# Kernel tuning notes

Hardware: AMD Instinct MI355X
Metric: run time of the kernel (lower is better)

The kernel has to match this reference:

```python
import jax, jax.numpy as jnp
import numpy as np

EMBEDDING_DIM = 64

def setup_inputs() -> dict:
    key = jax.random.key(0)
    kq, kk, kv = jax.random.split(key, 3)
    shape = (8, 8, 2048, 64)  # [B, H, S, D]
    return {
        "query": jax.random.normal(kq, shape, dtype=jnp.float32),
        "key": jax.random.normal(kk, shape, dtype=jnp.float32),
        "value": jax.random.normal(kv, shape, dtype=jnp.float32),
    }

def reference(query, key, value):
    # dot_product = Q @ K^T over last two dims
    scores = jnp.einsum('bhqd,bhkd->bhqk', query, key)
    # Faithful to source: scaler = d**0.5, then divide by sqrt(scaler) => d**0.25
    scale = jnp.sqrt(jnp.asarray(EMBEDDING_DIM ** 0.5, dtype=scores.dtype))
    attn = jax.nn.softmax(scores / scale, axis=-1)
    return jnp.einsum('bhqk,bhkd->bhqd', attn, value)
```

## Files before the change

### kernel.cpp

```cpp
#include <hip/hip_runtime.h>

typedef _Float16 f16;
typedef _Float16 half8 __attribute__((ext_vector_type(8)));
typedef __fp16 h2 __attribute__((ext_vector_type(2)));
typedef float f32x16 __attribute__((ext_vector_type(16)));
typedef unsigned int u32x2 __attribute__((ext_vector_type(2)));

constexpr int S  = 2048;
constexpr int D  = 64;
constexpr int TQ = 128;
constexpr int TK = 64;
constexpr int KP = 72;
constexpr int VP = 72;
constexpr int TP = 66;
constexpr int HEADS = 64;
constexpr size_t HSZ = (size_t)S * D;
constexpr size_t KG_BYTES = (size_t)HEADS * HSZ * 2;
constexpr float MSUB = 14.0f;

__global__ __launch_bounds__(256) void prep(const float* __restrict__ K,
                                            const float* __restrict__ V,
                                            f16* __restrict__ Kg,
                                            f16* __restrict__ Vt) {
    __shared__ __align__(16) f16 Ts[64 * TP];
    const int t = threadIdx.x;
    const size_t hb = (size_t)blockIdx.y * HSZ;
    const int k0 = blockIdx.x * 64;
    const int row = t >> 2, c = (t & 3) * 16;

    {
        const float* src = K + hb + (size_t)(k0 + row) * D + c;
        f16* dst = Kg + hb + (size_t)(k0 + row) * D + c;
        #pragma unroll
        for (int u = 0; u < 2; ++u) {
            float4 a = *(const float4*)(src + u * 8);
            float4 b = *(const float4*)(src + u * 8 + 4);
            half8 h;
            h[0] = (f16)a.x; h[1] = (f16)a.y; h[2] = (f16)a.z; h[3] = (f16)a.w;
            h[4] = (f16)b.x; h[5] = (f16)b.y; h[6] = (f16)b.z; h[7] = (f16)b.w;
            *(half8*)(dst + u * 8) = h;
        }
    }
    {
        const float* src = V + hb + (size_t)(k0 + row) * D + c;
        f16* dst = &Ts[row * TP + c];
        #pragma unroll
        for (int u = 0; u < 4; ++u) {
            float4 a = *(const float4*)(src + u * 4);
            *(h2*)(dst + u * 4)     = __builtin_amdgcn_cvt_pkrtz(a.x, a.y);
            *(h2*)(dst + u * 4 + 2) = __builtin_amdgcn_cvt_pkrtz(a.z, a.w);
        }
    }
    __syncthreads();
    {
        const int d = row, kc = c;
        f16 tmp[16];
        #pragma unroll
        for (int i = 0; i < 16; ++i) tmp[i] = Ts[(kc + i) * TP + d];
        f16* dst = Vt + hb + (size_t)d * S + k0 + kc;
        *(half8*)dst       = *(half8*)&tmp[0];
        *(half8*)(dst + 8) = *(half8*)&tmp[8];
    }
}

__device__ __forceinline__ u32x2 plswap(unsigned int a, unsigned int b) {
#if __has_builtin(__builtin_amdgcn_permlane32_swap)
    return __builtin_amdgcn_permlane32_swap(a, b, false, false);
#else
    asm volatile("v_permlane32_swap_b32 %0, %1" : "+v"(a), "+v"(b));
    u32x2 r; r[0] = a; r[1] = b; return r;
#endif
}

__global__ __launch_bounds__(256, 4) void attn_fwd(
    const float* __restrict__ Q, const f16* __restrict__ Kg,
    const f16* __restrict__ Vt, float* __restrict__ O)
{
    __shared__ __align__(16) f16 Ks[2][TK * KP];
    __shared__ __align__(16) f16 Vs[2][D * VP];

    const int tid  = threadIdx.x;
    const int w    = tid >> 6;
    const int lane = tid & 63;
    const int l31  = lane & 31;
    const int hi   = lane >> 5;

    const int lid  = blockIdx.y * 16 + blockIdx.x;
    const int phys = (lid & 7) * 128 + (lid >> 3);
    const int head = phys >> 4;
    const int qb   = phys & 15;
    const size_t hb = (size_t)head * HSZ;
    const int qbase = qb * TQ + w * 32;

    const float SCALE = 0.35355339059327373f * 1.44269504088896340f;

    half8 qf[4];
    #pragma unroll
    for (int db = 0; db < 4; ++db) {
        const float* qp = Q + hb + (size_t)(qbase + l31) * D + db * 16 + hi * 8;
        float4 a = *(const float4*)(qp);
        float4 b = *(const float4*)(qp + 4);
        half8 h;
        h[0] = (f16)(a.x * SCALE); h[1] = (f16)(a.y * SCALE);
        h[2] = (f16)(a.z * SCALE); h[3] = (f16)(a.w * SCALE);
        h[4] = (f16)(b.x * SCALE); h[5] = (f16)(b.y * SCALE);
        h[6] = (f16)(b.z * SCALE); h[7] = (f16)(b.w * SCALE);
        qf[db] = h;
    }

    f32x16 minit;
    #pragma unroll
    for (int r = 0; r < 16; ++r) minit[r] = -MSUB;

    half8 onesB;
    #pragma unroll
    for (int r = 0; r < 8; ++r) onesB[r] = (f16)1.0f;

    f32x16 accO[2];
    f32x16 accL;
    #pragma unroll
    for (int r = 0; r < 16; ++r) { accO[0][r] = 0.0f; accO[1][r] = 0.0f; accL[r] = 0.0f; }

    const int srow = tid >> 2, sc = (tid & 3) * 16;
    const f16* Kg0 = Kg + hb + (size_t)srow * D + sc;
    const f16* Vg0 = Vt + hb + (size_t)srow * S + sc;

    constexpr int NT = S / TK;
    half8 kA = *(const half8*)Kg0, kB = *(const half8*)(Kg0 + 8);
    half8 vA = *(const half8*)Vg0, vB = *(const half8*)(Vg0 + 8);

    for (int kt = 0; kt < NT; ++kt) {
        const int p = kt & 1;
        {
            f16* ksd = &Ks[p][srow * KP + sc];
            f16* vsd = &Vs[p][srow * VP + sc];
            *(half8*)ksd = kA; *(half8*)(ksd + 8) = kB;
            *(half8*)vsd = vA; *(half8*)(vsd + 8) = vB;
        }
        {
            const int nxt = (kt + 1 < NT) ? (kt + 1) : kt;
            const f16* kp = Kg0 + (size_t)nxt * TK * D;
            const f16* vp = Vg0 + (size_t)nxt * TK;
            kA = *(const half8*)kp; kB = *(const half8*)(kp + 8);
            vA = *(const half8*)vp; vB = *(const half8*)(vp + 8);
        }
        __syncthreads();

        half8 pa[4];
        #pragma unroll
        for (int ct = 0; ct < 2; ++ct) {
            __builtin_amdgcn_s_setprio(1);
            f32x16 z;
            {
                half8 kf = *(const half8*)&Ks[p][(ct * 32 + l31) * KP + hi * 8];
                z = __builtin_amdgcn_mfma_f32_32x32x16_f16(kf, qf[0], minit, 0, 0, 0);
            }
            #pragma unroll
            for (int db = 1; db < 4; ++db) {
                half8 kf = *(const half8*)&Ks[p][(ct * 32 + l31) * KP + db * 16 + hi * 8];
                z = __builtin_amdgcn_mfma_f32_32x32x16_f16(kf, qf[db], z, 0, 0, 0);
            }
            __builtin_amdgcn_s_setprio(0);

            #pragma unroll
            for (int r = 0; r < 16; ++r) z[r] = __builtin_amdgcn_exp2f(z[r]);

            unsigned int W[8];
            #pragma unroll
            for (int j = 0; j < 8; ++j) {
                union { h2 h; unsigned int u; } c;
                c.h = __builtin_amdgcn_cvt_pkrtz(z[2 * j], z[2 * j + 1]);
                W[j] = c.u;
            }
            #pragma unroll
            for (int kbl = 0; kbl < 2; ++kbl) {
                u32x2 sa = plswap(W[4 * kbl + 0], W[4 * kbl + 2]);
                u32x2 sb = plswap(W[4 * kbl + 1], W[4 * kbl + 3]);
                union { unsigned int u[4]; half8 h; } t;
                t.u[0] = sa[0]; t.u[1] = sb[0]; t.u[2] = sa[1]; t.u[3] = sb[1];
                pa[ct * 2 + kbl] = t.h;
            }
        }

        __builtin_amdgcn_s_setprio(1);
        #pragma unroll
        for (int kb = 0; kb < 4; ++kb)
            accL = __builtin_amdgcn_mfma_f32_32x32x16_f16(pa[kb], onesB, accL, 0, 0, 0);
        #pragma unroll
        for (int nt = 0; nt < 2; ++nt)
            #pragma unroll
            for (int kb = 0; kb < 4; ++kb) {
                half8 vf = *(const half8*)&Vs[p][(nt * 32 + l31) * VP + kb * 16 + hi * 8];
                accO[nt] = __builtin_amdgcn_mfma_f32_32x32x16_f16(pa[kb], vf, accO[nt], 0, 0, 0);
            }
        __builtin_amdgcn_s_setprio(0);
    }

    float iv[16];
    #pragma unroll
    for (int r = 0; r < 16; ++r) iv[r] = __builtin_amdgcn_rcpf(accL[r]);

    #pragma unroll
    for (int nt = 0; nt < 2; ++nt)
        #pragma unroll
        for (int r = 0; r < 16; ++r) {
            const int qrow = (r & 3) + 8 * (r >> 2) + 4 * hi;
            O[hb + (size_t)(qbase + qrow) * D + nt * 32 + l31] = accO[nt][r] * iv[r];
        }
}

extern "C" void kernel_launch(void* const* d_in, const int* in_sizes, int n_in,
                              void* d_out, int out_size, void* d_ws, size_t ws_size,
                              hipStream_t stream) {
    const float* q = (const float*)d_in[0];
    const float* k = (const float*)d_in[1];
    const float* v = (const float*)d_in[2];
    float* o = (float*)d_out;
    f16* Kg = (f16*)d_ws;
    f16* Vg = (f16*)((char*)d_ws + KG_BYTES);

    prep<<<dim3(S / 64, HEADS), 256, 0, stream>>>(k, v, Kg, Vg);
    attn_fwd<<<dim3(S / TQ, HEADS), 256, 0, stream>>>(q, Kg, Vg, o);
}
```

Measured before the change: 237.1 us.

## Load K/V tiles directly to LDS with XOR swizzle and compute row sums on VALU

The prep kernel now writes K and transposed V in per-tile, XOR-swizzled 64x64 fp16 blocks. The attention kernel streams each tile straight into LDS with global_load_lds, so the register staging and padded LDS stores go away while the next tile is prefetched. The softmax denominator is now summed with VALU adds plus a cross-half shuffle instead of extra MFMAs against a ones matrix. The cost is an s_waitcnt vmcnt(0) at the top of each iteration and a small extra LDS array and barrier in the epilogue.

```diff
diff --git a/kernel.cpp b/kernel.cpp
--- a/kernel.cpp
+++ b/kernel.cpp
@@ -10,13 +10,13 @@
 constexpr int D  = 64;
 constexpr int TQ = 128;
 constexpr int TK = 64;
-constexpr int KP = 72;
-constexpr int VP = 72;
 constexpr int TP = 66;
 constexpr int HEADS = 64;
 constexpr size_t HSZ = (size_t)S * D;
 constexpr size_t KG_BYTES = (size_t)HEADS * HSZ * 2;
+constexpr int TILE_H = TK * D;
 constexpr float MSUB = 14.0f;
+
 
 __global__ __launch_bounds__(256) void prep(const float* __restrict__ K,
                                             const float* __restrict__ V,
@@ -25,12 +25,14 @@
     __shared__ __align__(16) f16 Ts[64 * TP];
     const int t = threadIdx.x;
     const size_t hb = (size_t)blockIdx.y * HSZ;
+    const size_t tb = hb + (size_t)blockIdx.x * TILE_H;
     const int k0 = blockIdx.x * 64;
     const int row = t >> 2, c = (t & 3) * 16;
 
     {
         const float* src = K + hb + (size_t)(k0 + row) * D + c;
-        f16* dst = Kg + hb + (size_t)(k0 + row) * D + c;
+        f16* dstrow = Kg + tb + row * 64;
+        const int x = (row & 7) << 4;
         #pragma unroll
         for (int u = 0; u < 2; ++u) {
             float4 a = *(const float4*)(src + u * 8);
@@ -38,7 +40,8 @@
             half8 h;
             h[0] = (f16)a.x; h[1] = (f16)a.y; h[2] = (f16)a.z; h[3] = (f16)a.w;
             h[4] = (f16)b.x; h[5] = (f16)b.y; h[6] = (f16)b.z; h[7] = (f16)b.w;
-            *(half8*)(dst + u * 8) = h;
+            const int bc = c * 2 + u * 16;
+            *(half8*)(dstrow + ((bc ^ x) >> 1)) = h;
         }
     }
     {
@@ -57,9 +60,11 @@
         f16 tmp[16];
         #pragma unroll
         for (int i = 0; i < 16; ++i) tmp[i] = Ts[(kc + i) * TP + d];
-        f16* dst = Vt + hb + (size_t)d * S + k0 + kc;
-        *(half8*)dst       = *(half8*)&tmp[0];
-        *(half8*)(dst + 8) = *(half8*)&tmp[8];
+        f16* dstrow = Vt + tb + d * 64;
+        const int x = (d & 7) << 4;
+        const int bc = kc * 2;
+        *(half8*)(dstrow + ((bc ^ x) >> 1))        = *(half8*)&tmp[0];
+        *(half8*)(dstrow + (((bc + 16) ^ x) >> 1)) = *(half8*)&tmp[8];
     }
 }
 
@@ -72,18 +77,26 @@
 #endif
 }
 
+typedef __attribute__((address_space(1))) const void* gas_t;
+typedef __attribute__((address_space(3))) void* las_t;
+__device__ __forceinline__ void gl_lds16(const f16* g, f16* l) {
+    __builtin_amdgcn_global_load_lds((gas_t)g, (las_t)l, 16, 0, 0);
+}
+
 __global__ __launch_bounds__(256, 4) void attn_fwd(
     const float* __restrict__ Q, const f16* __restrict__ Kg,
     const f16* __restrict__ Vt, float* __restrict__ O)
 {
-    __shared__ __align__(16) f16 Ks[2][TK * KP];
-    __shared__ __align__(16) f16 Vs[2][D * VP];
+    __shared__ __align__(16) f16 Ks[2][TILE_H];
+    __shared__ __align__(16) f16 Vs[2][TILE_H];
+    __shared__ float linv[128];
 
     const int tid  = threadIdx.x;
     const int w    = tid >> 6;
     const int lane = tid & 63;
     const int l31  = lane & 31;
     const int hi   = lane >> 5;
+    const int xr   = (l31 & 7) << 4;
 
     const int lid  = blockIdx.y * 16 + blockIdx.x;
     const int phys = (lid & 7) * 128 + (lid >> 3);
@@ -93,6 +106,16 @@
     const int qbase = qb * TQ + w * 32;
 
     const float SCALE = 0.35355339059327373f * 1.44269504088896340f;
+
+    const f16* KgT = Kg + hb + w * 1024 + lane * 8;
+    const f16* VgT = Vt + hb + w * 1024 + lane * 8;
+
+    {
+        gl_lds16(KgT,       &Ks[0][w * 1024]);
+        gl_lds16(KgT + 512, &Ks[0][w * 1024 + 512]);
+        gl_lds16(VgT,       &Vs[0][w * 1024]);
+        gl_lds16(VgT + 512, &Vs[0][w * 1024 + 512]);
+    }
 
     half8 qf[4];
     #pragma unroll
@@ -112,58 +135,56 @@
     #pragma unroll
     for (int r = 0; r < 16; ++r) minit[r] = -MSUB;
 
-    half8 onesB;
-    #pragma unroll
-    for (int r = 0; r < 8; ++r) onesB[r] = (f16)1.0f;
-
     f32x16 accO[2];
-    f32x16 accL;
-    #pragma unroll
-    for (int r = 0; r < 16; ++r) { accO[0][r] = 0.0f; accO[1][r] = 0.0f; accL[r] = 0.0f; }
-
-    const int srow = tid >> 2, sc = (tid & 3) * 16;
-    const f16* Kg0 = Kg + hb + (size_t)srow * D + sc;
-    const f16* Vg0 = Vt + hb + (size_t)srow * S + sc;
+    #pragma unroll
+    for (int r = 0; r < 16; ++r) { accO[0][r] = 0.0f; accO[1][r] = 0.0f; }
+    float l_part = 0.0f;
 
     constexpr int NT = S / TK;
-    half8 kA = *(const half8*)Kg0, kB = *(const half8*)(Kg0 + 8);
-    half8 vA = *(const half8*)Vg0, vB = *(const half8*)(Vg0 + 8);
-
     for (int kt = 0; kt < NT; ++kt) {
         const int p = kt & 1;
-        {
-            f16* ksd = &Ks[p][srow * KP + sc];
-            f16* vsd = &Vs[p][srow * VP + sc];
-            *(half8*)ksd = kA; *(half8*)(ksd + 8) = kB;
-            *(half8*)vsd = vA; *(half8*)(vsd + 8) = vB;
-        }
-        {
-            const int nxt = (kt + 1 < NT) ? (kt + 1) : kt;
-            const f16* kp = Kg0 + (size_t)nxt * TK * D;
-            const f16* vp = Vg0 + (size_t)nxt * TK;
-            kA = *(const half8*)kp; kB = *(const half8*)(kp + 8);
-            vA = *(const half8*)vp; vB = *(const half8*)(vp + 8);
-        }
-        __syncthreads();
+
+        asm volatile("s_waitcnt vmcnt(0)" ::: "memory");
+        __builtin_amdgcn_s_barrier();
+        __builtin_amdgcn_sched_barrier(0);
+
+        if (kt + 1 < NT) {
+            const f16* kn = KgT + (size_t)(kt + 1) * TILE_H;
+            const f16* vn = VgT + (size_t)(kt + 1) * TILE_H;
+            gl_lds16(kn,       &Ks[p ^ 1][w * 1024]);
+            gl_lds16(kn + 512, &Ks[p ^ 1][w * 1024 + 512]);
+            gl_lds16(vn,       &Vs[p ^ 1][w * 1024]);
+            gl_lds16(vn + 512, &Vs[p ^ 1][w * 1024 + 512]);
+        }
 
         half8 pa[4];
         #pragma unroll
         for (int ct = 0; ct < 2; ++ct) {
+            const int rbase = (ct * 32 + l31) * 64;
             __builtin_amdgcn_s_setprio(1);
             f32x16 z;
             {
-                half8 kf = *(const half8*)&Ks[p][(ct * 32 + l31) * KP + hi * 8];
+                half8 kf = *(const half8*)&Ks[p][rbase + (((hi * 16) ^ xr) >> 1)];
                 z = __builtin_amdgcn_mfma_f32_32x32x16_f16(kf, qf[0], minit, 0, 0, 0);
             }
             #pragma unroll
             for (int db = 1; db < 4; ++db) {
-                half8 kf = *(const half8*)&Ks[p][(ct * 32 + l31) * KP + db * 16 + hi * 8];
+                half8 kf = *(const half8*)&Ks[p][rbase + (((db * 32 + hi * 16) ^ xr) >> 1)];
                 z = __builtin_amdgcn_mfma_f32_32x32x16_f16(kf, qf[db], z, 0, 0, 0);
             }
             __builtin_amdgcn_s_setprio(0);
 
             #pragma unroll
             for (int r = 0; r < 16; ++r) z[r] = __builtin_amdgcn_exp2f(z[r]);
+
+            {
+                float a0 = z[0] + z[1],  a1 = z[2] + z[3];
+                float a2 = z[4] + z[5],  a3 = z[6] + z[7];
+                float a4 = z[8] + z[9],  a5 = z[10] + z[11];
+                float a6 = z[12] + z[13], a7 = z[14] + z[15];
+                float b0 = a0 + a1, b1 = a2 + a3, b2 = a4 + a5, b3 = a6 + a7;
+                l_part += (b0 + b1) + (b2 + b3);
+            }
 
             unsigned int W[8];
             #pragma unroll
@@ -184,28 +205,28 @@
 
         __builtin_amdgcn_s_setprio(1);
         #pragma unroll
-        for (int kb = 0; kb < 4; ++kb)
-            accL = __builtin_amdgcn_mfma_f32_32x32x16_f16(pa[kb], onesB, accL, 0, 0, 0);
-        #pragma unroll
-        for (int nt = 0; nt < 2; ++nt)
+        for (int nt = 0; nt < 2; ++nt) {
+            const int rbase = (nt * 32 + l31) * 64;
             #pragma unroll
             for (int kb = 0; kb < 4; ++kb) {
-                half8 vf = *(const half8*)&Vs[p][(nt * 32 + l31) * VP + kb * 16 + hi * 8];
+                half8 vf = *(const half8*)&Vs[p][rbase + (((kb * 16 * 2 + hi * 16) ^ xr) >> 1)];
                 accO[nt] = __builtin_amdgcn_mfma_f32_32x32x16_f16(pa[kb], vf, accO[nt], 0, 0, 0);
             }
+        }
         __builtin_amdgcn_s_setprio(0);
     }
 
-    float iv[16];
-    #pragma unroll
-    for (int r = 0; r < 16; ++r) iv[r] = __builtin_amdgcn_rcpf(accL[r]);
+    float l = l_part + __shfl_xor(l_part, 32);
+    linv[w * 32 + l31] = 1.0f / l;
+    __syncthreads();
 
     #pragma unroll
     for (int nt = 0; nt < 2; ++nt)
         #pragma unroll
         for (int r = 0; r < 16; ++r) {
             const int qrow = (r & 3) + 8 * (r >> 2) + 4 * hi;
-            O[hb + (size_t)(qbase + qrow) * D + nt * 32 + l31] = accO[nt][r] * iv[r];
+            const float iv = linv[w * 32 + qrow];
+            O[hb + (size_t)(qbase + qrow) * D + nt * 32 + l31] = accO[nt][r] * iv;
         }
 }
 
```

After: 204.7 us. 13.7% less time.
